# Performance work log

Measured on AMD Instinct MI355X. Metric: run time of the kernel, lower is better.

The kernel has to match this reference:

```python
import jax, jax.numpy as jnp
import numpy as np

H = 16
D_MODEL = 1024
D_K = D_MODEL // H
B, S = 4, 2048


def setup_inputs() -> dict:
    key = jax.random.key(0)
    ks = jax.random.split(key, 12)
    scale = 1.0 / np.sqrt(D_MODEL)
    inp = {
        "query": jax.random.normal(ks[0], (B, S, D_MODEL), jnp.float32),
        "key_in": jax.random.normal(ks[1], (B, S, D_MODEL), jnp.float32),
        "value": jax.random.normal(ks[2], (B, S, D_MODEL), jnp.float32),
        "mask": jax.random.randint(ks[3], (B, 1, S, S), 0, 2, jnp.int32),
    }
    # 4 Linear(d_model, d_model) layers: Wq, Wk, Wv, Wo (+ biases)
    names = ["q", "k", "v", "o"]
    for i, n in enumerate(names):
        inp[f"W{n}"] = jax.random.normal(ks[4 + i], (D_MODEL, D_MODEL), jnp.float32) * scale
        inp[f"b{n}"] = jax.random.normal(ks[8 + i], (D_MODEL,), jnp.float32) * scale
    return inp


def reference(query, key_in, value, mask, Wq, bq, Wk, bk, Wv, bv, Wo, bo):
    # Linear projections then split heads: [B,S,D] -> [B,H,S,Dk]
    def proj(x, W, b):
        y = jnp.einsum("bsd,ed->bse", x, W) + b  # torch Linear: x @ W.T + b
        return y.reshape(B, S, H, D_K).transpose(0, 2, 1, 3)

    q = proj(query, Wq, bq)
    k = proj(key_in, Wk, bk)
    v = proj(value, Wv, bv)

    scores = jnp.einsum("bhqd,bhkd->bhqk", q, k) / jnp.sqrt(jnp.float32(D_K))
    scores = jnp.where(mask == 0, jnp.float32(-1e9), scores)
    p_attn = jax.nn.softmax(scores, axis=-1)
    # dropout is identity in eval mode
    x = jnp.einsum("bhqk,bhkd->bhqd", p_attn, v)
    x = x.transpose(0, 2, 1, 3).reshape(B, S, D_MODEL)
    return jnp.einsum("bsd,ed->bse", x, Wo) + bo
```

## Files before the change

### kernel.cpp

```cpp
#include <hip/hip_runtime.h>
#include <hip/hip_bf16.h>

typedef __bf16 bf16_t;
typedef __attribute__((ext_vector_type(8))) __bf16 bf16x8;
typedef __attribute__((ext_vector_type(4))) __bf16 bf16x4;
typedef __attribute__((ext_vector_type(4))) float f32x4;
typedef __attribute__((ext_vector_type(16))) float f32x16;

#define GAS __attribute__((address_space(1)))
#define LAS __attribute__((address_space(3)))

__device__ __forceinline__ void async_copy16(const bf16_t* g, bf16_t* l) {
    __builtin_amdgcn_global_load_lds((const GAS void*)g, (LAS void*)l, 16, 0, 0);
}

__global__ __launch_bounds__(256) void convert_kernel(
    const float* __restrict__ src, bf16_t* __restrict__ dst, int n)
{
    int i = (blockIdx.x * 256 + threadIdx.x) * 8;
    if (i >= n) return;
    f32x4 f0 = *(const f32x4*)(src + i);
    f32x4 f1 = *(const f32x4*)(src + i + 4);
    bf16x8 v;
#pragma unroll
    for (int j = 0; j < 4; j++) { v[j] = (bf16_t)f0[j]; v[4 + j] = (bf16_t)f1[j]; }
    *(bf16x8*)&dst[i] = v;
}

__global__ __launch_bounds__(256) void pack_mask_kernel(
    const int* __restrict__ mask, unsigned long long* __restrict__ out)
{
    int i = blockIdx.x * 256 + threadIdx.x;
    unsigned long long bits = __ballot(mask[i] != 0);
    if ((threadIdx.x & 63) == 0) out[i >> 6] = bits;
}

template<int MODE>
__global__ __launch_bounds__(256, 2) void gemm_nt(
    const bf16_t* __restrict__ A, const bf16_t* __restrict__ W,
    const float* __restrict__ bias, void* __restrict__ out_, float oscale)
{
    __shared__ __align__(16) bf16_t Als[128 * 32];
    __shared__ __align__(16) bf16_t Bls[128 * 32];

    const int tid  = threadIdx.x;
    const int wave = tid >> 6, lane = tid & 63;
    const int quad = lane >> 4, lq = lane & 15;
    const int wm = wave >> 1, wn = wave & 1;
    const int tm = blockIdx.x * 128, tn = blockIdx.y * 128;
    const int K = 1024;

    const bf16_t* gA0 = A + (size_t)(tm + wave * 32 + (lane >> 2)) * K + (lane & 3) * 8;
    const bf16_t* gA1 = gA0 + (size_t)16 * K;
    const bf16_t* gB0 = W + (size_t)(tn + wave * 32 + (lane >> 2)) * K + (lane & 3) * 8;
    const bf16_t* gB1 = gB0 + (size_t)16 * K;
    bf16_t* lA0 = &Als[(wave * 32) * 32];
    bf16_t* lA1 = &Als[(wave * 32 + 16) * 32];
    bf16_t* lB0 = &Bls[(wave * 32) * 32];
    bf16_t* lB1 = &Bls[(wave * 32 + 16) * 32];

    f32x4 acc[4][4] = {};

    for (int k0 = 0; k0 < K; k0 += 32) {
        __syncthreads();
        async_copy16(gA0, lA0);
        async_copy16(gA1, lA1);
        async_copy16(gB0, lB0);
        async_copy16(gB1, lB1);
        gA0 += 32; gA1 += 32; gB0 += 32; gB1 += 32;
        __syncthreads();

        bf16x8 af[4], bfr[4];
#pragma unroll
        for (int i = 0; i < 4; i++) {
            af[i]  = *(const bf16x8*)&Als[(wm * 64 + i * 16 + lq) * 32 + quad * 8];
            bfr[i] = *(const bf16x8*)&Bls[(wn * 64 + i * 16 + lq) * 32 + quad * 8];
        }
#pragma unroll
        for (int i = 0; i < 4; i++)
#pragma unroll
            for (int j = 0; j < 4; j++) {
                if (MODE == 2)
                    acc[i][j] = __builtin_amdgcn_mfma_f32_16x16x32_bf16(bfr[j], af[i], acc[i][j], 0, 0, 0);
                else
                    acc[i][j] = __builtin_amdgcn_mfma_f32_16x16x32_bf16(af[i], bfr[j], acc[i][j], 0, 0, 0);
            }
    }

    float* outf = (float*)out_;
    bf16_t* outb = (bf16_t*)out_;
#pragma unroll
    for (int i = 0; i < 4; i++)
#pragma unroll
        for (int j = 0; j < 4; j++)
#pragma unroll
            for (int r = 0; r < 4; r++) {
                float v = acc[i][j][r];
                if (MODE == 0) {
                    int row = tm + wm * 64 + i * 16 + quad * 4 + r;
                    int col = tn + wn * 64 + j * 16 + lq;
                    outf[(size_t)row * 1024 + col] = (v + bias[col]) * oscale;
                } else if (MODE == 1) {
                    int row = tm + wm * 64 + i * 16 + quad * 4 + r;
                    int col = tn + wn * 64 + j * 16 + lq;
                    v = (v + bias[col]) * oscale;
                    int b = row >> 11, s = row & 2047;
                    int h = col >> 6,  dk = col & 63;
                    outb[(((size_t)(b * 16 + h) * 2048 + s) << 6) + dk] = (bf16_t)v;
                } else {
                    int n = tn + wn * 64 + j * 16 + quad * 4 + r;
                    int m = tm + wm * 64 + i * 16 + lq;
                    v = (v + bias[n]) * oscale;
                    int b = m >> 11, s = m & 2047;
                    int h = n >> 6,  dk = n & 63;
                    outb[((size_t)((b * 16 + h) * 64 + dk) << 11) + s] = (bf16_t)v;
                }
            }
}

#define LDK 72
#define LDV 72
#define LDP 68

__global__ __launch_bounds__(256, 2) void attn_kernel(
    const bf16_t* __restrict__ Q, const bf16_t* __restrict__ Kh,
    const bf16_t* __restrict__ Vt, const unsigned int* __restrict__ mp,
    bf16_t* __restrict__ X)
{
    __shared__ __align__(16) bf16_t Kls[64 * LDK];
    __shared__ __align__(16) bf16_t Vls[64 * LDV];
    __shared__ __align__(16) bf16_t Pls[4][64 * LDP];

    const int tid  = threadIdx.x;
    const int wave = tid >> 6, lane = tid & 63;
    const int l31  = lane & 31;
    const int hi8  = (lane >> 5) * 8, hi4 = (lane >> 5) * 4;
    const int xr8  = lane & 8;
    const int bh = blockIdx.y;
    const int b  = bh >> 4, h = bh & 15;
    const int qb = blockIdx.x * 256 + wave * 64;

    bf16x8 qf[2][4];
#pragma unroll
    for (int qg = 0; qg < 2; qg++) {
        const bf16_t* qp = Q + ((size_t)bh * 2048 + qb + qg * 32 + l31) * 64 + hi8;
#pragma unroll
        for (int c = 0; c < 4; c++) qf[qg][c] = *(const bf16x8*)(qp + c * 16);
    }

    f32x16 od[2][2] = {};
    float lsum[2] = {0.f, 0.f};

    const int sr = tid >> 3, sc = tid & 7;
    const bf16_t* gK0 = Kh + ((size_t)bh * 2048 + sr) * 64 + sc * 8;
    const bf16_t* gK1 = gK0 + 32 * 64;
    const bf16_t* gV0 = Vt + ((size_t)bh * 64 + sr) * 2048 + sc * 8;
    const bf16_t* gV1 = gV0 + 32 * 2048;
    const int swc = (sc * 8) ^ (sr & 8);
    bf16_t* lK0 = &Kls[sr * LDK + swc];
    bf16_t* lK1 = &Kls[(sr + 32) * LDK + swc];
    bf16_t* lV0 = &Vls[sr * LDV + swc];
    bf16_t* lV1 = &Vls[(sr + 32) * LDV + swc];

    const unsigned long long* mq0 =
        (const unsigned long long*)mp + ((size_t)(b << 11) + qb + l31) * 32;
    const unsigned long long* mq1 = mq0 + 32 * 32;

    bf16x8 ks0 = *(const bf16x8*)gK0, ks1 = *(const bf16x8*)gK1;
    bf16x8 vs0 = *(const bf16x8*)gV0, vs1 = *(const bf16x8*)gV1;

    bf16_t* pw = &Pls[wave][0];

    for (int kt = 0; kt < 32; kt++) {
        __syncthreads();
        *(bf16x8*)lK0 = ks0; *(bf16x8*)lK1 = ks1;
        *(bf16x8*)lV0 = vs0; *(bf16x8*)lV1 = vs1;
        __syncthreads();
        if (kt < 31) {
            gK0 += 4096; gK1 += 4096; gV0 += 64; gV1 += 64;
            ks0 = *(const bf16x8*)gK0; ks1 = *(const bf16x8*)gK1;
            vs0 = *(const bf16x8*)gV0; vs1 = *(const bf16x8*)gV1;
        }
        unsigned long long mw[2] = { mq0[kt], mq1[kt] };

#pragma unroll
        for (int kh = 0; kh < 2; kh++) {
            bf16x8 kf[4];
            const bf16_t* krow = &Kls[(kh * 32 + l31) * LDK];
#pragma unroll
            for (int c = 0; c < 4; c++)
                kf[c] = *(const bf16x8*)(krow + ((c * 16 + hi8) ^ xr8));

#pragma unroll
            for (int qg = 0; qg < 2; qg++) {
                f32x16 z = {};
                z = __builtin_amdgcn_mfma_f32_32x32x16_bf16(kf[0], qf[qg][0], z, 0, 0, 0);
                z = __builtin_amdgcn_mfma_f32_32x32x16_bf16(kf[1], qf[qg][1], z, 0, 0, 0);
                z = __builtin_amdgcn_mfma_f32_32x32x16_bf16(kf[2], qf[qg][2], z, 0, 0, 0);
                z = __builtin_amdgcn_mfma_f32_32x32x16_bf16(kf[3], qf[qg][3], z, 0, 0, 0);
                unsigned int mbits = (unsigned int)(mw[qg] >> (kh * 32 + hi4));
                float ls = 0.f;
#pragma unroll
                for (int p = 0; p < 4; p++) {
                    bf16x4 pk;
#pragma unroll
                    for (int r = 0; r < 4; r++) {
                        float sv = ((mbits >> (8 * p + r)) & 1) ? z[4 * p + r] : -1e9f;
                        float e = __expf(sv);
                        ls += e;
                        pk[r] = (bf16_t)e;
                    }
                    *(bf16x4*)&pw[(qg * 32 + l31) * LDP + kh * 32 + 8 * p + hi4] = pk;
                }
                lsum[qg] += ls;
            }

            bf16x8 pf[2][2];
#pragma unroll
            for (int qg = 0; qg < 2; qg++) {
                const bf16_t* prow = &pw[(qg * 32 + l31) * LDP + kh * 32 + hi8];
                pf[qg][0] = *(const bf16x8*)(prow);
                pf[qg][1] = *(const bf16x8*)(prow + 16);
            }
#pragma unroll
            for (int c = 0; c < 2; c++)
#pragma unroll
                for (int dt = 0; dt < 2; dt++) {
                    bf16x8 vf = *(const bf16x8*)&Vls[(dt * 32 + l31) * LDV +
                                                     ((kh * 32 + c * 16 + hi8) ^ xr8)];
                    od[0][dt] = __builtin_amdgcn_mfma_f32_32x32x16_bf16(vf, pf[0][c], od[0][dt], 0, 0, 0);
                    od[1][dt] = __builtin_amdgcn_mfma_f32_32x32x16_bf16(vf, pf[1][c], od[1][dt], 0, 0, 0);
                }
        }
    }

#pragma unroll
    for (int qg = 0; qg < 2; qg++) {
        float l = lsum[qg] + __shfl_xor(lsum[qg], 32);
        float rl = (l > 0.f) ? 1.0f / l : 0.f;
        int qrow = qb + qg * 32 + l31;
        bf16_t* xp = X + ((size_t)(b * 2048) + qrow) * 1024 + h * 64 + hi4;
#pragma unroll
        for (int dt = 0; dt < 2; dt++)
#pragma unroll
            for (int p = 0; p < 4; p++) {
                bf16x4 ov;
#pragma unroll
                for (int r = 0; r < 4; r++)
                    ov[r] = (bf16_t)(od[qg][dt][p * 4 + r] * rl);
                *(bf16x4*)(xp + dt * 32 + p * 8) = ov;
            }
    }
}

extern "C" void kernel_launch(void* const* d_in, const int* in_sizes, int n_in,
                              void* d_out, int out_size, void* d_ws, size_t ws_size,
                              hipStream_t stream)
{
    const float* query  = (const float*)d_in[0];
    const float* key_in = (const float*)d_in[1];
    const float* value  = (const float*)d_in[2];
    const int*   mask   = (const int*)d_in[3];

    char* ws = (char*)d_ws;
    const size_t SZ  = (size_t)8192 * 1024 * 2;
    const size_t MPK = (size_t)2 * 1024 * 1024;
    const size_t WSZ = (size_t)1024 * 1024 * 2;
    bf16_t* C   = (bf16_t*)(ws);
    bf16_t* Qb  = (bf16_t*)(ws + SZ);
    bf16_t* Kb  = (bf16_t*)(ws + 2 * SZ);
    bf16_t* Vtb = (bf16_t*)(ws + 3 * SZ);
    unsigned long long* mpack = (unsigned long long*)(ws + 4 * SZ);
    bf16_t* Wc[4];
    for (int i = 0; i < 4; i++)
        Wc[i] = (bf16_t*)(ws + 4 * SZ + MPK + i * WSZ);

    const size_t NEED = 4 * SZ + MPK + 4 * WSZ;
    if (ws_size < NEED) return;

    const int NACT = 8192 * 1024;
    for (int i = 0; i < 4; i++)
        convert_kernel<<<512, 256, 0, stream>>>((const float*)d_in[4 + 2 * i],
                                                Wc[i], 1024 * 1024);
    pack_mask_kernel<<<65536, 256, 0, stream>>>(mask, mpack);

    dim3 gg(64, 8);
    convert_kernel<<<4096, 256, 0, stream>>>(query, C, NACT);
    gemm_nt<1><<<gg, 256, 0, stream>>>(C, Wc[0], (const float*)d_in[5], Qb, 0.125f);
    convert_kernel<<<4096, 256, 0, stream>>>(key_in, C, NACT);
    gemm_nt<1><<<gg, 256, 0, stream>>>(C, Wc[1], (const float*)d_in[7], Kb, 1.0f);
    convert_kernel<<<4096, 256, 0, stream>>>(value, C, NACT);
    gemm_nt<2><<<gg, 256, 0, stream>>>(C, Wc[2], (const float*)d_in[9], Vtb, 1.0f);

    attn_kernel<<<dim3(8, 64), 256, 0, stream>>>(Qb, Kb, Vtb,
                                                 (const unsigned int*)mpack, C);
    gemm_nt<0><<<gg, 256, 0, stream>>>(C, Wc[3], (const float*)d_in[11], d_out, 1.0f);
}
```

Measured before the change: 469.4 us.

## Load K/V fragments directly from global in single-wave attention blocks

The attention kernel changes from 256-thread blocks that stage K and V tiles in shared memory behind two barriers per tile into 64-thread single-wave blocks. Each wave reads its K and V MFMA fragments straight from global memory, relying on L2/L1 caching. The P-times-V step is moved into a separate loop after both softmax halves are written. This removes the barriers and LDS staging, but the four waves that used to share each K/V tile now fetch it separately, multiplying global/cache traffic, and there is no software prefetch to hide load latency.

```diff
diff --git a/kernel.cpp b/kernel.cpp
--- a/kernel.cpp
+++ b/kernel.cpp
@@ -118,27 +118,21 @@
             }
 }
 
-#define LDK 72
-#define LDV 72
 #define LDP 68
 
-__global__ __launch_bounds__(256, 2) void attn_kernel(
+__global__ __launch_bounds__(64, 2) void attn_kernel(
     const bf16_t* __restrict__ Q, const bf16_t* __restrict__ Kh,
     const bf16_t* __restrict__ Vt, const unsigned int* __restrict__ mp,
     bf16_t* __restrict__ X)
 {
-    __shared__ __align__(16) bf16_t Kls[64 * LDK];
-    __shared__ __align__(16) bf16_t Vls[64 * LDV];
-    __shared__ __align__(16) bf16_t Pls[4][64 * LDP];
-
-    const int tid  = threadIdx.x;
-    const int wave = tid >> 6, lane = tid & 63;
+    __shared__ __align__(16) bf16_t Pls[64 * LDP];
+
+    const int lane = threadIdx.x;
     const int l31  = lane & 31;
     const int hi8  = (lane >> 5) * 8, hi4 = (lane >> 5) * 4;
-    const int xr8  = lane & 8;
     const int bh = blockIdx.y;
     const int b  = bh >> 4, h = bh & 15;
-    const int qb = blockIdx.x * 256 + wave * 64;
+    const int qb = blockIdx.x * 64;
 
     bf16x8 qf[2][4];
 #pragma unroll
@@ -151,45 +145,27 @@
     f32x16 od[2][2] = {};
     float lsum[2] = {0.f, 0.f};
 
-    const int sr = tid >> 3, sc = tid & 7;
-    const bf16_t* gK0 = Kh + ((size_t)bh * 2048 + sr) * 64 + sc * 8;
-    const bf16_t* gK1 = gK0 + 32 * 64;
-    const bf16_t* gV0 = Vt + ((size_t)bh * 64 + sr) * 2048 + sc * 8;
-    const bf16_t* gV1 = gV0 + 32 * 2048;
-    const int swc = (sc * 8) ^ (sr & 8);
-    bf16_t* lK0 = &Kls[sr * LDK + swc];
-    bf16_t* lK1 = &Kls[(sr + 32) * LDK + swc];
-    bf16_t* lV0 = &Vls[sr * LDV + swc];
-    bf16_t* lV1 = &Vls[(sr + 32) * LDV + swc];
+    const bf16_t* kbase = Kh + ((size_t)bh * 2048 + l31) * 64 + hi8;
+    const bf16_t* vb0   = Vt + ((size_t)bh * 64 + l31) * 2048 + hi8;
+    const bf16_t* vb1   = vb0 + (size_t)32 * 2048;
 
     const unsigned long long* mq0 =
         (const unsigned long long*)mp + ((size_t)(b << 11) + qb + l31) * 32;
     const unsigned long long* mq1 = mq0 + 32 * 32;
 
-    bf16x8 ks0 = *(const bf16x8*)gK0, ks1 = *(const bf16x8*)gK1;
-    bf16x8 vs0 = *(const bf16x8*)gV0, vs1 = *(const bf16x8*)gV1;
-
-    bf16_t* pw = &Pls[wave][0];
+    bf16_t* pw = &Pls[0];
 
     for (int kt = 0; kt < 32; kt++) {
-        __syncthreads();
-        *(bf16x8*)lK0 = ks0; *(bf16x8*)lK1 = ks1;
-        *(bf16x8*)lV0 = vs0; *(bf16x8*)lV1 = vs1;
-        __syncthreads();
-        if (kt < 31) {
-            gK0 += 4096; gK1 += 4096; gV0 += 64; gV1 += 64;
-            ks0 = *(const bf16x8*)gK0; ks1 = *(const bf16x8*)gK1;
-            vs0 = *(const bf16x8*)gV0; vs1 = *(const bf16x8*)gV1;
-        }
         unsigned long long mw[2] = { mq0[kt], mq1[kt] };
+        const bf16_t* kk = kbase + (size_t)(kt * 64) * 64;
 
 #pragma unroll
         for (int kh = 0; kh < 2; kh++) {
             bf16x8 kf[4];
-            const bf16_t* krow = &Kls[(kh * 32 + l31) * LDK];
+            const bf16_t* krow = kk + (size_t)(kh * 32) * 64;
 #pragma unroll
             for (int c = 0; c < 4; c++)
-                kf[c] = *(const bf16x8*)(krow + ((c * 16 + hi8) ^ xr8));
+                kf[c] = *(const bf16x8*)(krow + c * 16);
 
 #pragma unroll
             for (int qg = 0; qg < 2; qg++) {
@@ -214,7 +190,10 @@
                 }
                 lsum[qg] += ls;
             }
-
+        }
+
+#pragma unroll
+        for (int kh = 0; kh < 2; kh++) {
             bf16x8 pf[2][2];
 #pragma unroll
             for (int qg = 0; qg < 2; qg++) {
@@ -222,15 +201,16 @@
                 pf[qg][0] = *(const bf16x8*)(prow);
                 pf[qg][1] = *(const bf16x8*)(prow + 16);
             }
-#pragma unroll
-            for (int c = 0; c < 2; c++)
-#pragma unroll
-                for (int dt = 0; dt < 2; dt++) {
-                    bf16x8 vf = *(const bf16x8*)&Vls[(dt * 32 + l31) * LDV +
-                                                     ((kh * 32 + c * 16 + hi8) ^ xr8)];
-                    od[0][dt] = __builtin_amdgcn_mfma_f32_32x32x16_bf16(vf, pf[0][c], od[0][dt], 0, 0, 0);
-                    od[1][dt] = __builtin_amdgcn_mfma_f32_32x32x16_bf16(vf, pf[1][c], od[1][dt], 0, 0, 0);
-                }
+            const size_t voff = (size_t)(kt * 64 + kh * 32);
+#pragma unroll
+            for (int c = 0; c < 2; c++) {
+                bf16x8 vf0 = *(const bf16x8*)(vb0 + voff + c * 16);
+                bf16x8 vf1 = *(const bf16x8*)(vb1 + voff + c * 16);
+                od[0][0] = __builtin_amdgcn_mfma_f32_32x32x16_bf16(vf0, pf[0][c], od[0][0], 0, 0, 0);
+                od[1][0] = __builtin_amdgcn_mfma_f32_32x32x16_bf16(vf0, pf[1][c], od[1][0], 0, 0, 0);
+                od[0][1] = __builtin_amdgcn_mfma_f32_32x32x16_bf16(vf1, pf[0][c], od[0][1], 0, 0, 0);
+                od[1][1] = __builtin_amdgcn_mfma_f32_32x32x16_bf16(vf1, pf[1][c], od[1][1], 0, 0, 0);
+            }
         }
     }
 
@@ -292,7 +272,7 @@
     convert_kernel<<<4096, 256, 0, stream>>>(value, C, NACT);
     gemm_nt<2><<<gg, 256, 0, stream>>>(C, Wc[2], (const float*)d_in[9], Vtb, 1.0f);
 
-    attn_kernel<<<dim3(8, 64), 256, 0, stream>>>(Qb, Kb, Vtb,
+    attn_kernel<<<dim3(32, 64), 64, 0, stream>>>(Qb, Kb, Vtb,
                                                  (const unsigned int*)mpack, C);
     gemm_nt<0><<<gg, 256, 0, stream>>>(C, Wc[3], (const float*)d_in[11], d_out, 1.0f);
 }
```

New measurement: 486.6 us. +3.7%, slower.
